# Kernel optimization log

Hardware: AMD Instinct MI355X
Metric: run time of the kernel (lower is better)

Reference implementation:

```python
import jax, jax.numpy as jnp
import numpy as np

K = 30          # hard-coded in Hypergraph.from_feature_kNN(ft, k=30)
BN_EPS = 1e-5   # BatchNorm1d eval mode, running_mean=0, running_var=1


def setup_inputs() -> dict:
    key = jax.random.key(0)
    ks = jax.random.split(key, 3)
    B, C, H, W = 8, 64, 56, 56
    hid = 32
    return {
        "x": jax.random.normal(ks[0], (B, C, H, W), jnp.float32),
        "w1": jax.random.normal(ks[1], (C, hid), jnp.float32) / np.sqrt(C).astype(np.float32),
        "b1": jnp.zeros((hid,), jnp.float32),
        "g1": jnp.ones((hid,), jnp.float32),
        "be1": jnp.zeros((hid,), jnp.float32),
        "w2": jax.random.normal(ks[2], (hid, C), jnp.float32) / np.sqrt(hid).astype(np.float32),
        "b2": jnp.zeros((C,), jnp.float32),
        "g2": jnp.ones((C,), jnp.float32),
        "be2": jnp.zeros((C,), jnp.float32),
    }


def _knn_idx(ft, k):
    # squared euclidean distances via gram trick; same ordering as torch.cdist
    sq = jnp.sum(ft * ft, axis=1)
    d2 = sq[:, None] + sq[None, :] - 2.0 * (ft @ ft.T)   # [L, L]
    _, idx = jax.lax.top_k(-d2, k)                        # k smallest distances (incl. self)
    return idx                                            # [L, k] -> hyperedge e = kNN of vertex e


def _v2v_mean(X, nbr):
    # hg.v2v(X, aggr="mean"): v2e mean then e2v mean over the kNN incidence structure
    L, k = nbr.shape
    F = X.shape[1]
    Y = jnp.mean(X[nbr], axis=1)                                        # v2e: [L_edges, F]
    seg = nbr.reshape(-1)                                               # vertex nbr[e,j] belongs to edge e
    vals = jnp.broadcast_to(Y[:, None, :], (L, k, F)).reshape(L * k, F)
    s = jax.ops.segment_sum(vals, seg, num_segments=L)                  # e2v sum
    dv = jax.ops.segment_sum(jnp.ones((L * k,), X.dtype), seg, num_segments=L)
    return s / jnp.maximum(dv, 1.0)[:, None]                            # e2v mean


def _bn_eval(x, g, b):
    # BatchNorm1d in eval: running_mean=0, running_var=1
    return x * (g * np.float32(1.0 / np.sqrt(1.0 + BN_EPS))) + b


def reference(x, w1, b1, g1, be1, w2, b2, g2, be2):
    B, C, H, W = x.shape
    L = H * W
    xf = x.reshape(B, L, C)  # faithful raw x.view(B, L, C) (no transpose in source)

    def per_sample(ft):
        nbr = _knn_idx(ft, K)
        # HGNNPConv 1: theta -> bn -> v2v(mean) -> relu (dropout off in eval)
        h = _bn_eval(ft @ w1 + b1, g1, be1)
        h = jax.nn.relu(_v2v_mean(h, nbr))
        # HGNNPConv 2 (is_last): theta -> bn -> v2v(mean), no act/drop
        h = _bn_eval(h @ w2 + b2, g2, be2)
        return _v2v_mean(h, nbr)  # [L, C]

    outs = jax.vmap(per_sample)(xf)      # [B, L, C]
    return outs.reshape(B, -1, H, W)     # faithful raw outs.view(B, -1, H, W)
```

## Files before the change

### kernel.cpp

```cpp
#include <hip/hip_runtime.h>
#include <math.h>


namespace {

constexpr int cB = 8;
constexpr int cL = 3136;
constexpr int cC = 64;
constexpr int cH = 32;
constexpr int cK = 30;
constexpr int NV = cB * cL;
constexpr int QD = 10;
constexpr float BN_SC = 0.99999500003749964f;

typedef __bf16 bf16x4 __attribute__((ext_vector_type(4)));
typedef __bf16 bf16x8 __attribute__((ext_vector_type(8)));
typedef float floatx4 __attribute__((ext_vector_type(4)));

__device__ inline unsigned umin2(unsigned a, unsigned b) { return a < b ? a : b; }
__device__ inline unsigned umax2(unsigned a, unsigned b) { return a > b ? a : b; }
__device__ inline unsigned umin3(unsigned a, unsigned b, unsigned c) {
  return umin2(umin2(a, b), c);
}
__device__ inline float bf16lo(unsigned u) { return __uint_as_float(u << 16); }
__device__ inline float bf16hi(unsigned u) {
  return __uint_as_float(u & 0xFFFF0000u);
}

__device__ inline unsigned bclean64(unsigned v, int ln) {
#pragma unroll
  for (int off = 32; off; off >>= 1) {
    unsigned p = (unsigned)__shfl_xor((int)v, off);
    v = (ln & off) ? umax2(v, p) : umin2(v, p);
  }
  return v;
}

__global__ void k_split(const float* __restrict__ x, ushort* __restrict__ xhi,
                        ushort* __restrict__ xlo, float* __restrict__ sqf,
                        int* __restrict__ cnt, int* __restrict__ cur) {
  int v = blockIdx.x * 256 + threadIdx.x;
  if (v >= NV) return;
  cnt[v] = 0;
  cur[v] = 0;
  const float4* p = reinterpret_cast<const float4*>(x) + (size_t)v * 16;
  double s = 0.0;
#pragma unroll
  for (int c = 0; c < 16; ++c) {
    float4 f = p[c];
    bf16x4 hh, ll;
#pragma unroll
    for (int e = 0; e < 4; ++e) {
      float a = (&f.x)[e];
      __bf16 h = (__bf16)a;
      ll[e] = (__bf16)(a - (float)h);
      hh[e] = h;
      s += (double)a * (double)a;
    }
    *reinterpret_cast<bf16x4*>(&xhi[(size_t)v * 64 + c * 4]) = hh;
    *reinterpret_cast<bf16x4*>(&xlo[(size_t)v * 64 + c * 4]) = ll;
  }
  sqf[v] = (float)(s * 64.0 + 32768.0);
}

__global__ __launch_bounds__(128, 4) void k_sweep(
    const ushort* __restrict__ xhi, const ushort* __restrict__ xlo,
    const float* __restrict__ sqf, unsigned* __restrict__ candq) {
  const int ib = blockIdx.x, qt = blockIdx.y, b = blockIdx.z;
  const int r0 = ib * 32;
  const int jb0 = qt * 1568;
  const int ntile = 49;
  const size_t bbase = (size_t)b * cL;

  __shared__ ushort aHi[32 * 72], aLo[32 * 72];
  __shared__ ushort bHi[32 * 72], bLo[32 * 72];
  __shared__ float sqJs[32];

  const int t  = threadIdx.x;
  const int ln = t & 63;
  const int w  = t >> 6;
  const int tx = ln & 15;
  const int qd = ln >> 4;

#pragma unroll
  for (int it = 0; it < 2; ++it) {
    int idx = t + 128 * it;
    int r = idx >> 3, blk = idx & 7;
    *reinterpret_cast<uint4*>(&aHi[r * 72 + blk * 8]) =
        *reinterpret_cast<const uint4*>(&xhi[(bbase + r0 + r) * 64 + blk * 8]);
    *reinterpret_cast<uint4*>(&aLo[r * 72 + blk * 8]) =
        *reinterpret_cast<const uint4*>(&xlo[(bbase + r0 + r) * 64 + blk * 8]);
  }
  __syncthreads();

  bf16x8 aH[2], aL[2];
#pragma unroll
  for (int kk = 0; kk < 2; ++kk) {
    aH[kk] = *reinterpret_cast<const bf16x8*>(
        &aHi[(w * 16 + tx) * 72 + kk * 32 + qd * 8]);
    aL[kk] = *reinterpret_cast<const bf16x8*>(
        &aLo[(w * 16 + tx) * 72 + kk * 32 + qd * 8]);
  }

  unsigned q[4][QD];
#pragma unroll
  for (int e = 0; e < 4; ++e)
#pragma unroll
    for (int k = 0; k < QD; ++k) q[e][k] = 0xFFFFFFFFu;

  const int pr  = (t + 0)   >> 3, pblk  = (t + 0)   & 7;
  const int pr1 = (t + 128) >> 3, pblk1 = (t + 128) & 7;
  uint4 pH0, pH1, pL0, pL1;
  float pS = 0.f;
  {
    const int jb = jb0;
    pH0 = *reinterpret_cast<const uint4*>(&xhi[(bbase + jb + pr) * 64 + pblk * 8]);
    pL0 = *reinterpret_cast<const uint4*>(&xlo[(bbase + jb + pr) * 64 + pblk * 8]);
    pH1 = *reinterpret_cast<const uint4*>(&xhi[(bbase + jb + pr1) * 64 + pblk1 * 8]);
    pL1 = *reinterpret_cast<const uint4*>(&xlo[(bbase + jb + pr1) * 64 + pblk1 * 8]);
    if (t < 32) pS = sqf[bbase + jb + t];
  }

  for (int st = 0; st < ntile; ++st) {
    __syncthreads();
    *reinterpret_cast<uint4*>(&bHi[pr * 72 + pblk * 8])   = pH0;
    *reinterpret_cast<uint4*>(&bLo[pr * 72 + pblk * 8])   = pL0;
    *reinterpret_cast<uint4*>(&bHi[pr1 * 72 + pblk1 * 8]) = pH1;
    *reinterpret_cast<uint4*>(&bLo[pr1 * 72 + pblk1 * 8]) = pL1;
    if (t < 32) sqJs[t] = pS;
    __syncthreads();

    if (st + 1 < ntile) {
      const int jb = jb0 + (st + 1) * 32;
      pH0 = *reinterpret_cast<const uint4*>(&xhi[(bbase + jb + pr) * 64 + pblk * 8]);
      pL0 = *reinterpret_cast<const uint4*>(&xlo[(bbase + jb + pr) * 64 + pblk * 8]);
      pH1 = *reinterpret_cast<const uint4*>(&xhi[(bbase + jb + pr1) * 64 + pblk1 * 8]);
      pL1 = *reinterpret_cast<const uint4*>(&xlo[(bbase + jb + pr1) * 64 + pblk1 * 8]);
      if (t < 32) pS = sqf[bbase + jb + t];
    }
    __builtin_amdgcn_sched_barrier(0);

    unsigned pk[2][4];
#pragma unroll
    for (int f = 0; f < 2; ++f) {
      const int bro = (f * 16 + tx) * 72 + qd * 8;
      bf16x8 bh0 = *reinterpret_cast<const bf16x8*>(&bHi[bro]);
      bf16x8 bh1 = *reinterpret_cast<const bf16x8*>(&bHi[bro + 32]);
      bf16x8 bl0 = *reinterpret_cast<const bf16x8*>(&bLo[bro]);
      bf16x8 bl1 = *reinterpret_cast<const bf16x8*>(&bLo[bro + 32]);
      floatx4 acc = {0.f, 0.f, 0.f, 0.f};
      acc = __builtin_amdgcn_mfma_f32_16x16x32_bf16(aH[0], bh0, acc, 0, 0, 0);
      acc = __builtin_amdgcn_mfma_f32_16x16x32_bf16(aH[1], bh1, acc, 0, 0, 0);
      acc = __builtin_amdgcn_mfma_f32_16x16x32_bf16(aH[0], bl0, acc, 0, 0, 0);
      acc = __builtin_amdgcn_mfma_f32_16x16x32_bf16(aH[1], bl1, acc, 0, 0, 0);
      acc = __builtin_amdgcn_mfma_f32_16x16x32_bf16(aL[0], bh0, acc, 0, 0, 0);
      acc = __builtin_amdgcn_mfma_f32_16x16x32_bf16(aL[1], bh1, acc, 0, 0, 0);
      const float sjs = sqJs[f * 16 + tx];
      const unsigned col = (unsigned)(jb0 + st * 32 + f * 16 + tx);
#pragma unroll
      for (int e = 0; e < 4; ++e) {
        float qf = fmaf(acc[e], -128.f, sjs);
        qf = fminf(fmaxf(qf, 0.f), 65535.f);
        pk[f][e] = ((unsigned)qf << 12) | col;
      }
    }

#pragma unroll
    for (int e = 0; e < 4; ++e) {
      unsigned a0 = umin2(pk[0][e], pk[1][e]);
      unsigned a1 = umax2(pk[0][e], pk[1][e]);
#pragma unroll
      for (int i = QD - 1; i >= 2; --i)
        q[e][i] = umin3(q[e][i], umax2(q[e][i - 1], a0),
                        umax2(q[e][i - 2], a1));
      q[e][1] = umin3(q[e][1], umax2(q[e][0], a0), a1);
      q[e][0] = umin3(q[e][0], a0, a1);
    }
  }

  unsigned* cr[4];
#pragma unroll
  for (int e = 0; e < 4; ++e)
    cr[e] = candq + (bbase + r0 + w * 16 + qd * 4 + e) * 80 + qt * 40;
  for (int it = 0; it < 40; ++it) {
    unsigned h0 = q[0][0], h1 = q[1][0], h2 = q[2][0], h3 = q[3][0];
    unsigned m0 = h0, m1 = h1, m2 = h2, m3 = h3;
#pragma unroll
    for (int off = 1; off < 16; off <<= 1) {
      m0 = umin2(m0, (unsigned)__shfl_xor((int)m0, off));
      m1 = umin2(m1, (unsigned)__shfl_xor((int)m1, off));
      m2 = umin2(m2, (unsigned)__shfl_xor((int)m2, off));
      m3 = umin2(m3, (unsigned)__shfl_xor((int)m3, off));
    }
    if (tx == 0) {
      cr[0][it] = m0;
      cr[1][it] = m1;
      cr[2][it] = m2;
      cr[3][it] = m3;
    }
    if (h0 == m0) {
#pragma unroll
      for (int k = 0; k < QD - 1; ++k) q[0][k] = q[0][k + 1];
      q[0][QD - 1] = 0xFFFFFFFFu;
    }
    if (h1 == m1) {
#pragma unroll
      for (int k = 0; k < QD - 1; ++k) q[1][k] = q[1][k + 1];
      q[1][QD - 1] = 0xFFFFFFFFu;
    }
    if (h2 == m2) {
#pragma unroll
      for (int k = 0; k < QD - 1; ++k) q[2][k] = q[2][k + 1];
      q[2][QD - 1] = 0xFFFFFFFFu;
    }
    if (h3 == m3) {
#pragma unroll
      for (int k = 0; k < QD - 1; ++k) q[3][k] = q[3][k + 1];
      q[3][QD - 1] = 0xFFFFFFFFu;
    }
  }
}

__global__ __launch_bounds__(256) void k_rescore(const float* __restrict__ x,
                                                 const unsigned* __restrict__ candq,
                                                 int* __restrict__ nbr,
                                                 int* __restrict__ cnt) {
  const int w  = threadIdx.x >> 6;
  const int ln = threadIdx.x & 63;
  const size_t row = (size_t)blockIdx.x * 4 + w;
  const size_t bvert = row - (row % cL);

  const unsigned* cq = candq + row * 80;
  unsigned A = (ln < 40) ? cq[ln]      : 0xFFFFFFFFu;
  unsigned B = (ln < 40) ? cq[40 + ln] : 0xFFFFFFFFu;

  unsigned g = umin2(A, (unsigned)__shfl((int)B, 63 - ln));
  g = bclean64(g, ln);

  const unsigned qv = g >> 12;
  const int col = min((int)(g & 0xFFFu), cL - 1);

  unsigned q29 = (unsigned)__shfl((int)qv, 29);
  unsigned q30 = (unsigned)__shfl((int)qv, 30);
  if (q30 > q29 + 3) {
    if (ln < cK) {
      nbr[row * cK + ln] = col;
      atomicAdd(&cnt[bvert + col], 1);
    }
    return;
  }

  float4 xi[16];
  const float4* xi4 = reinterpret_cast<const float4*>(x + row * 64);
#pragma unroll
  for (int c = 0; c < 16; ++c) xi[c] = xi4[c];

  double dv = 1e300;
  if (ln < 40) {
    const float4* xj4 = reinterpret_cast<const float4*>(x + (bvert + col) * 64);
    double ax = 0.0, ay = 0.0, az = 0.0, aw = 0.0;
#pragma unroll
    for (int c = 0; c < 16; ++c) {
      float4 xj = xj4[c];
      double d0 = (double)xi[c].x - (double)xj.x; ax = fma(d0, d0, ax);
      double d1 = (double)xi[c].y - (double)xj.y; ay = fma(d1, d1, ay);
      double d2 = (double)xi[c].z - (double)xj.z; az = fma(d2, d2, az);
      double d3 = (double)xi[c].w - (double)xj.w; aw = fma(d3, d3, aw);
    }
    dv = (ax + ay) + (az + aw);
  }
  int r2 = 0;
  for (int j = 0; j < 40; ++j) {
    double od = __shfl(dv, j);
    r2 += (od < dv || (od == dv && j < ln)) ? 1 : 0;
  }
  if (ln < 40 && r2 < cK) {
    nbr[row * cK + r2] = col;
    atomicAdd(&cnt[bvert + col], 1);
  }
}

__global__ __launch_bounds__(1024) void k_scan(const int* __restrict__ cnt,
                                               int* __restrict__ rp) {
  const int b = blockIdx.x;
  const int* c = cnt + b * cL;
  int* r = rp + b * (cL + 1);
  const int t = threadIdx.x;
  const int ln = t & 63, w = t >> 6;

  int v[4];
  int s = 0;
#pragma unroll
  for (int i = 0; i < 4; ++i) {
    int idx = 4 * t + i;
    v[i] = (idx < cL) ? c[idx] : 0;
    s += v[i];
  }
  int inc = s;
#pragma unroll
  for (int off = 1; off < 64; off <<= 1) {
    int u = __shfl_up(inc, off);
    if (ln >= off) inc += u;
  }
  __shared__ int wsum[16];
  if (ln == 63) wsum[w] = inc;
  __syncthreads();
  int carry = 0;
#pragma unroll
  for (int i = 0; i < 16; ++i) carry += (i < w) ? wsum[i] : 0;

  int excl = carry + inc - s;
#pragma unroll
  for (int i = 0; i < 4; ++i) {
    int idx = 4 * t + i;
    if (idx < cL) r[idx] = excl;
    excl += v[i];
  }
  if (t == 1023) r[cL] = excl;
}

__global__ void k_fill(const int* __restrict__ nbr, const int* __restrict__ rp,
                       int* __restrict__ cur, int* __restrict__ el) {
  int g = blockIdx.x * 256 + threadIdx.x;
  if (g >= NV * cK) return;
  int b = g / (cL * cK);
  int e = (g / cK) % cL;
  int v = nbr[g];
  v = min(max(v, 0), cL - 1);
  int p = rp[b * (cL + 1) + v] + atomicAdd(&cur[b * cL + v], 1);
  p = min(max(p, 0), cL * cK - 1);
  el[(size_t)b * cL * cK + p] = e;
}

__global__ __launch_bounds__(256) void k_theta1(const float* __restrict__ x,
                                                const float* __restrict__ w1,
                                                const float* __restrict__ b1,
                                                const float* __restrict__ g1,
                                                const float* __restrict__ be1,
                                                __bf16* __restrict__ h1) {
  __shared__ float w[cC * cH];
  int t = threadIdx.x;
  for (int n = t; n < cC * cH; n += 256) w[n] = w1[n];
  __syncthreads();
  int g = blockIdx.x * 256 + t;
  int row = g >> 5;
  int f = g & 31;
  const float4* xr = reinterpret_cast<const float4*>(x) + (size_t)row * 16;
  float s = 0.f;
#pragma unroll
  for (int kc = 0; kc < 16; ++kc) {
    float4 xv = xr[kc];
    s += xv.x * w[(4 * kc + 0) * cH + f];
    s += xv.y * w[(4 * kc + 1) * cH + f];
    s += xv.z * w[(4 * kc + 2) * cH + f];
    s += xv.w * w[(4 * kc + 3) * cH + f];
  }
  h1[g] = (__bf16)((s + b1[f]) * (g1[f] * BN_SC) + be1[f]);
}

__global__ __launch_bounds__(256) void k_v2e32(const __bf16* __restrict__ X,
                                               const int* __restrict__ nbr,
                                               __bf16* __restrict__ Y) {
  const int w  = threadIdx.x >> 6;
  const int ln = threadIdx.x & 63;
  const size_t er = (size_t)blockIdx.x * 4 + w;
  const size_t b  = er / cL;
  const __bf16* Xb = X + b * cL * cH;
  const int nb_l = nbr[er * cK + (ln < cK ? ln : cK - 1)];
  const int hi = ln >> 5, f = ln & 31;
  int idx[15];
#pragma unroll
  for (int m = 0; m < 15; ++m) idx[m] = __shfl(nb_l, hi + 2 * m);
  float y[15];
#pragma unroll
  for (int m = 0; m < 15; ++m) y[m] = (float)Xb[(size_t)idx[m] * cH + f];
  float s = 0.f;
#pragma unroll
  for (int m = 0; m < 15; ++m) s += y[m];
  s += __shfl_xor(s, 32);
  if (hi == 0) Y[er * cH + f] = (__bf16)(s * (1.f / 30.f));
}

__global__ __launch_bounds__(256) void k_e2v_t2(const __bf16* __restrict__ Y,
                                                const int* __restrict__ rp,
                                                const int* __restrict__ el,
                                                const float* __restrict__ w2,
                                                const float* __restrict__ b2,
                                                const float* __restrict__ g2,
                                                const float* __restrict__ be2,
                                                __bf16* __restrict__ h2) {
  __shared__ float w2s[cH * cC];
  {
    int t = threadIdx.x;
    for (int n = t; n < cH * cC; n += 256) w2s[n] = w2[n];
  }
  const int w  = threadIdx.x >> 6;
  const int ln = threadIdx.x & 63;
  const size_t vr = (size_t)blockIdx.x * 4 + w;
  const size_t b  = vr / cL;
  const int v = (int)(vr % cL);
  const int* rpb = rp + b * (cL + 1);
  const int s0 = rpb[v];
  const int deg = rpb[v + 1] - s0;
  const int* elb = el + b * (size_t)cL * cK + s0;
  const __bf16* Yb = Y + b * cL * cH;
  const int hi = ln >> 5, f = ln & 31;
  float s = 0.f;

  for (int base = 0; base < deg; base += 64) {
    const int take = min(64, deg - base);
    const int eidx = elb[base + (ln < take ? ln : 0)];
    for (int j0 = 0; j0 < take; j0 += 16) {
      float acc = 0.f;
#pragma unroll
      for (int k2 = 0; k2 < 8; ++k2) {
        int j = j0 + 2 * k2 + hi;
        int e0 = __shfl(eidx, j < take ? j : 0);
        float y = (float)Yb[(size_t)e0 * cH + f];
        acc += (j < take) ? y : 0.f;
      }
      s += acc;
    }
  }
  __syncthreads();

  s += __shfl_xor(s, 32);
  float r = fmaxf(s / (float)deg, 0.f);

  float s2 = 0.f;
#pragma unroll 8
  for (int k = 0; k < cH; ++k) {
    float rk = __shfl(r, k);
    s2 = fmaf(rk, w2s[k * cC + ln], s2);
  }
  h2[vr * cC + ln] = (__bf16)((s2 + b2[ln]) * (g2[ln] * BN_SC) + be2[ln]);
}

__global__ __launch_bounds__(256) void k_v2e64(const __bf16* __restrict__ X,
                                               const int* __restrict__ nbr,
                                               __bf16* __restrict__ Y) {
  const int w  = threadIdx.x >> 6;
  const int ln = threadIdx.x & 63;
  const size_t er = (size_t)blockIdx.x * 4 + w;
  const size_t b  = er / cL;
  const unsigned* Xb = reinterpret_cast<const unsigned*>(X + b * cL * cC);
  const int nb_l = nbr[er * cK + (ln < cK ? ln : cK - 1)];
  const int half = ln >> 5, f2 = ln & 31;
  int idx[15];
#pragma unroll
  for (int m = 0; m < 15; ++m) idx[m] = __shfl(nb_l, 2 * m + half);
  unsigned v[15];
#pragma unroll
  for (int m = 0; m < 15; ++m) v[m] = Xb[(size_t)idx[m] * 32 + f2];
  float s0 = 0.f, s1 = 0.f;
#pragma unroll
  for (int m = 0; m < 15; ++m) {
    s0 += bf16lo(v[m]);
    s1 += bf16hi(v[m]);
  }
  s0 += __shfl_xor(s0, 32);
  s1 += __shfl_xor(s1, 32);
  if (half == 0) {
    union {
      __bf16 h[2];
      unsigned u;
    } cv;
    cv.h[0] = (__bf16)(s0 * (1.f / 30.f));
    cv.h[1] = (__bf16)(s1 * (1.f / 30.f));
    reinterpret_cast<unsigned*>(Y)[er * 32 + f2] = cv.u;
  }
}

__global__ __launch_bounds__(256) void k_e2v64(const __bf16* __restrict__ Y,
                                               const int* __restrict__ rp,
                                               const int* __restrict__ el,
                                               float* __restrict__ out) {
  const int w  = threadIdx.x >> 6;
  const int ln = threadIdx.x & 63;
  const size_t vr = (size_t)blockIdx.x * 4 + w;
  const size_t b  = vr / cL;
  const int v = (int)(vr % cL);
  const int* rpb = rp + b * (cL + 1);
  const int s0r = rpb[v];
  const int deg = rpb[v + 1] - s0r;
  const int* elb = el + b * (size_t)cL * cK + s0r;
  const unsigned* Yb = reinterpret_cast<const unsigned*>(Y + b * cL * cC);
  const int half = ln >> 5, f2 = ln & 31;
  float s0 = 0.f, s1 = 0.f;

  for (int base = 0; base < deg; base += 64) {
    const int take = min(64, deg - base);
    const int eidx = elb[base + (ln < take ? ln : 0)];
    for (int j0 = 0; j0 < take; j0 += 16) {
      float a0 = 0.f, a1 = 0.f;
#pragma unroll
      for (int k2 = 0; k2 < 8; ++k2) {
        int j = j0 + 2 * k2 + half;
        int e0 = __shfl(eidx, j < take ? j : 0);
        unsigned u = Yb[(size_t)e0 * 32 + f2];
        bool ok = j < take;
        a0 += ok ? bf16lo(u) : 0.f;
        a1 += ok ? bf16hi(u) : 0.f;
      }
      s0 += a0;
      s1 += a1;
    }
  }
  s0 += __shfl_xor(s0, 32);
  s1 += __shfl_xor(s1, 32);
  float v0 = __shfl(s0, ln >> 1);
  float v1 = __shfl(s1, ln >> 1);
  out[vr * cC + ln] = ((ln & 1) ? v1 : v0) / (float)deg;
}

}

extern "C" void kernel_launch(void* const* d_in, const int* in_sizes, int n_in,
                              void* d_out, int out_size, void* d_ws,
                              size_t ws_size, hipStream_t stream) {
  (void)in_sizes; (void)n_in; (void)out_size; (void)ws_size;
  const float* x   = (const float*)d_in[0];
  const float* w1  = (const float*)d_in[1];
  const float* b1  = (const float*)d_in[2];
  const float* g1  = (const float*)d_in[3];
  const float* be1 = (const float*)d_in[4];
  const float* w2  = (const float*)d_in[5];
  const float* b2  = (const float*)d_in[6];
  const float* g2  = (const float*)d_in[7];
  const float* be2 = (const float*)d_in[8];
  float* out = (float*)d_out;

  char* base = (char*)d_ws;
  size_t off = 0;
  auto carve = [&](size_t bytes) {
    char* p = base + off;
    off += (bytes + 255) & ~(size_t)255;
    return p;
  };
  float* sqf = (float*)carve((size_t)NV * 4);
  int*   nbr = (int*)carve((size_t)NV * cK * 4);
  int*   rp  = (int*)carve((size_t)cB * (cL + 1) * 4);
  int*   cnt = (int*)carve((size_t)NV * 4);
  int*   cur = (int*)carve((size_t)NV * 4);
  char* RA = carve((size_t)NV * 64 * 2 * 2);
  ushort* xhi = (ushort*)RA;
  ushort* xlo = (ushort*)(RA + 3211264);
  int* el = (int*)RA;
  char* RC = carve((size_t)NV * 160 * 4);
  unsigned* candq = (unsigned*)RC;
  __bf16* h1 = (__bf16*)RC;
  __bf16* Y1 = (__bf16*)(RC + 1605632);
  __bf16* h2 = (__bf16*)(RC + 3211264);
  __bf16* Y2 = (__bf16*)(RC + 6422528);

  k_split<<<(NV + 255) / 256, 256, 0, stream>>>(x, xhi, xlo, sqf, cnt, cur);
  k_sweep<<<dim3(98, 2, cB), 128, 0, stream>>>(xhi, xlo, sqf, candq);
  k_rescore<<<NV / 4, 256, 0, stream>>>(x, candq, nbr, cnt);

  k_scan<<<cB, 1024, 0, stream>>>(cnt, rp);
  k_fill<<<(NV * cK) / 256, 256, 0, stream>>>(nbr, rp, cur, el);

  k_theta1<<<NV * cH / 256, 256, 0, stream>>>(x, w1, b1, g1, be1, h1);
  k_v2e32<<<NV / 4, 256, 0, stream>>>(h1, nbr, Y1);
  k_e2v_t2<<<NV / 4, 256, 0, stream>>>(Y1, rp, el, w2, b2, g2, be2, h2);
  k_v2e64<<<NV / 4, 256, 0, stream>>>(h2, nbr, Y2);
  k_e2v64<<<NV / 4, 256, 0, stream>>>(Y2, rp, el, out);
}
```

Baseline: 392.9 us.

## Refine kNN distance quantization, skip no-op queue updates, vectorize v2e gather

Raises the fixed-point scale of quantized distances from 16 to 20 bits, widening the ambiguity margin before falling back to exact recheck. Wraps the per-row sorted-queue insertion in a wave-wide __any test so tiles with no closer candidate skip the min/max network. Rewrites the v2e gather to load packed bf16 pairs as 32-bit words, with four neighbours per pass and shuffle reductions. The branch adds divergence checks, and the finer quantization changes how often the exact fallback path is taken.

```diff
diff --git a/kernel.cpp b/kernel.cpp
--- a/kernel.cpp
+++ b/kernel.cpp
@@ -60,7 +60,7 @@
     *reinterpret_cast<bf16x4*>(&xhi[(size_t)v * 64 + c * 4]) = hh;
     *reinterpret_cast<bf16x4*>(&xlo[(size_t)v * 64 + c * 4]) = ll;
   }
-  sqf[v] = (float)(s * 64.0 + 32768.0);
+  sqf[v] = (float)(s * 1024.0 + 262144.0);
 }
 
 __global__ __launch_bounds__(128, 4) void k_sweep(
@@ -159,8 +159,8 @@
       const unsigned col = (unsigned)(jb0 + st * 32 + f * 16 + tx);
 #pragma unroll
       for (int e = 0; e < 4; ++e) {
-        float qf = fmaf(acc[e], -128.f, sjs);
-        qf = fminf(fmaxf(qf, 0.f), 65535.f);
+        float qf = fmaf(acc[e], -2048.f, sjs);
+        qf = fminf(fmaxf(qf, 0.f), 1048575.f);
         pk[f][e] = ((unsigned)qf << 12) | col;
       }
     }
@@ -169,12 +169,14 @@
     for (int e = 0; e < 4; ++e) {
       unsigned a0 = umin2(pk[0][e], pk[1][e]);
       unsigned a1 = umax2(pk[0][e], pk[1][e]);
-#pragma unroll
-      for (int i = QD - 1; i >= 2; --i)
-        q[e][i] = umin3(q[e][i], umax2(q[e][i - 1], a0),
-                        umax2(q[e][i - 2], a1));
-      q[e][1] = umin3(q[e][1], umax2(q[e][0], a0), a1);
-      q[e][0] = umin3(q[e][0], a0, a1);
+      if (__any(a0 < q[e][QD - 1])) {
+#pragma unroll
+        for (int i = QD - 1; i >= 2; --i)
+          q[e][i] = umin3(q[e][i], umax2(q[e][i - 1], a0),
+                          umax2(q[e][i - 2], a1));
+        q[e][1] = umin3(q[e][1], umax2(q[e][0], a0), a1);
+        q[e][0] = umin3(q[e][0], a0, a1);
+      }
     }
   }
 
@@ -242,7 +244,7 @@
 
   unsigned q29 = (unsigned)__shfl((int)qv, 29);
   unsigned q30 = (unsigned)__shfl((int)qv, 30);
-  if (q30 > q29 + 3) {
+  if (q30 > q29 + 6) {
     if (ln < cK) {
       nbr[row * cK + ln] = col;
       atomicAdd(&cnt[bvert + col], 1);
@@ -365,20 +367,36 @@
   const int ln = threadIdx.x & 63;
   const size_t er = (size_t)blockIdx.x * 4 + w;
   const size_t b  = er / cL;
-  const __bf16* Xb = X + b * cL * cH;
+  const unsigned* Xb = reinterpret_cast<const unsigned*>(X + b * cL * cH);
   const int nb_l = nbr[er * cK + (ln < cK ? ln : cK - 1)];
-  const int hi = ln >> 5, f = ln & 31;
-  int idx[15];
-#pragma unroll
-  for (int m = 0; m < 15; ++m) idx[m] = __shfl(nb_l, hi + 2 * m);
-  float y[15];
-#pragma unroll
-  for (int m = 0; m < 15; ++m) y[m] = (float)Xb[(size_t)idx[m] * cH + f];
-  float s = 0.f;
-#pragma unroll
-  for (int m = 0; m < 15; ++m) s += y[m];
-  s += __shfl_xor(s, 32);
-  if (hi == 0) Y[er * cH + f] = (__bf16)(s * (1.f / 30.f));
+  const int qg = ln >> 4, f2 = ln & 15;
+  unsigned u[8];
+#pragma unroll
+  for (int m = 0; m < 8; ++m) {
+    int j = m * 4 + qg;
+    int idx = __shfl(nb_l, j < cK ? j : 0);
+    u[m] = Xb[(size_t)idx * 16 + f2];
+  }
+  float s0 = 0.f, s1 = 0.f;
+#pragma unroll
+  for (int m = 0; m < 8; ++m) {
+    bool ok = (m * 4 + qg) < cK;
+    s0 += ok ? bf16lo(u[m]) : 0.f;
+    s1 += ok ? bf16hi(u[m]) : 0.f;
+  }
+  s0 += __shfl_xor(s0, 16);
+  s1 += __shfl_xor(s1, 16);
+  s0 += __shfl_xor(s0, 32);
+  s1 += __shfl_xor(s1, 32);
+  if (ln < 16) {
+    union {
+      __bf16 h[2];
+      unsigned u;
+    } cv;
+    cv.h[0] = (__bf16)(s0 * (1.f / 30.f));
+    cv.h[1] = (__bf16)(s1 * (1.f / 30.f));
+    reinterpret_cast<unsigned*>(Y)[er * 16 + f2] = cv.u;
+  }
 }
 
 __global__ __launch_bounds__(256) void k_e2v_t2(const __bf16* __restrict__ Y,
```

Measured after the change: 389.7 us. No clear change (-0.8%).
